# Optimization experiments

Hardware: AMD Instinct MI355X
Metric: run time of the kernel (lower is better)

Reference implementation:

```python
import jax, jax.numpy as jnp
import numpy as np

N_NODES = 50000
N_EDGES = 800000
D = 128


def _gcn_conv(x, edge_index, W, b):
    """PyG GCNConv: out = D^{-1/2} (A + I) D^{-1/2} (x W) + b.

    edge_index[0] = source nodes, edge_index[1] = target nodes.
    Self-loops handled analytically instead of materializing them.
    """
    n = x.shape[0]
    src, dst = edge_index[0], edge_index[1]
    h = x @ W  # [N, out]
    # degree with self-loop: in-degree of target + 1
    deg = jax.ops.segment_sum(jnp.ones_like(dst, dtype=h.dtype), dst, num_segments=n) + 1.0
    dinv = jax.lax.rsqrt(deg)  # deg >= 1, safe
    norm = dinv[src] * dinv[dst]  # [E]
    msgs = norm[:, None] * h[src]  # [E, out]  (the big irregular-gather intermediate)
    agg = jax.ops.segment_sum(msgs, dst, num_segments=n)
    # self-loop contribution: norm = dinv[i]*dinv[i] = 1/deg
    agg = agg + h * (1.0 / deg)[:, None]
    return agg + b


def setup_inputs() -> dict:
    key = jax.random.key(0)
    k1, k2, k3, k4 = jax.random.split(key, 4)
    x = jax.random.normal(k1, (N_NODES, D), dtype=jnp.float32)
    edge_index = jax.random.randint(k2, (2, N_EDGES), 0, N_NODES, dtype=jnp.int64)
    scale = 1.0 / np.sqrt(D)
    W1 = jax.random.normal(k3, (D, D), dtype=jnp.float32) * scale
    W2 = jax.random.normal(k4, (D, D), dtype=jnp.float32) * scale
    b1 = jnp.zeros((D,), dtype=jnp.float32)
    b2 = jnp.zeros((D,), dtype=jnp.float32)
    return {"x": x, "edge_index": edge_index, "W1": W1, "b1": b1, "W2": W2, "b2": b2}


def reference(x, edge_index, W1, b1, W2, b2):
    h = _gcn_conv(x, edge_index, W1, b1)
    h = jax.nn.relu(h)  # dropout p=0.0 -> identity
    out = _gcn_conv(h, edge_index, W2, b2)
    return out
```

## Files before the change

### kernel.cpp

```cpp
#include <hip/hip_runtime.h>

#define DF 128
#define NBKT_MAX 256
#define CAP 8192

typedef unsigned int uint;
typedef unsigned short ushort;
typedef __attribute__((ext_vector_type(8))) short short8;
typedef __attribute__((ext_vector_type(4))) float f32x4;

union frag_u { uint4 u4; short8 s8; };

__device__ __forceinline__ uint f2u(float f) { return __float_as_uint(f); }
__device__ __forceinline__ ushort rne_bf16(float v) {
    uint u = __float_as_uint(v);
    u = u + 0x7FFFu + ((u >> 16) & 1u);
    return (ushort)(u >> 16);
}
__device__ __forceinline__ float bflo(uint u) { return __uint_as_float(u << 16); }
__device__ __forceinline__ float bfhi(uint u) { return __uint_as_float(u & 0xFFFF0000u); }

__global__ __launch_bounds__(256) void scatter_wprep(const int* __restrict__ src,
                                                     const int* __restrict__ dst,
                                                     int* __restrict__ ccur,
                                                     uint* __restrict__ ebuf,
                                                     int E, int NB, int SB,
                                                     const float* __restrict__ W1,
                                                     const float* __restrict__ W2,
                                                     uint4* __restrict__ Whi,
                                                     uint4* __restrict__ Wlo) {
    __shared__ int cnt[NBKT_MAX];
    __shared__ int base[NBKT_MAX];
    int t = threadIdx.x;
    if ((int)blockIdx.x < SB) {
        int e0 = blockIdx.x * 8192, e1 = min(E, e0 + 8192);
        for (int i = t; i < NB; i += 256) cnt[i] = 0;
        __syncthreads();
        for (int e = e0 + t; e < e1; e += 256) atomicAdd(&cnt[dst[e] >> 8], 1);
        __syncthreads();
        for (int i = t; i < NB; i += 256) base[i] = cnt[i] ? atomicAdd(&ccur[i], cnt[i]) : 0;
        __syncthreads();
        for (int e = e0 + t; e < e1; e += 256) {
            int d = dst[e];
            int b = d >> 8;
            int pos = atomicAdd(&base[b], 1);
            if (pos < CAP) ebuf[(size_t)b * CAP + pos] = ((uint)(d & 255) << 24) | (uint)src[e];
        }
    } else {
        int tt4 = ((int)blockIdx.x - SB) * 256 + t;
        int wsel = tt4 >> 11;
        int tt = tt4 & 2047;
        const float* W = wsel ? W2 : W1;
        int lane = tt & 63;
        int n  = ((tt >> 6) & 7) * 16 + (lane & 15);
        int k0 = (tt >> 9) * 32 + (lane >> 4) * 8;
        uint hi[4], lo[4];
#pragma unroll
        for (int p = 0; p < 4; ++p) {
            float f0 = W[(size_t)(k0 + 2 * p) * DF + n];
            float f1 = W[(size_t)(k0 + 2 * p + 1) * DF + n];
            uint u0 = f2u(f0), u1 = f2u(f1);
            hi[p] = (u1 & 0xFFFF0000u) | (u0 >> 16);
            float l0 = f0 - __uint_as_float(u0 & 0xFFFF0000u);
            float l1 = f1 - __uint_as_float(u1 & 0xFFFF0000u);
            lo[p] = (f2u(l1) & 0xFFFF0000u) | (f2u(l0) >> 16);
        }
        Whi[wsel * 2048 + tt] = make_uint4(hi[0], hi[1], hi[2], hi[3]);
        Wlo[wsel * 2048 + tt] = make_uint4(lo[0], lo[1], lo[2], lo[3]);
    }
}

__global__ __launch_bounds__(256) void bucket_sort(const uint* __restrict__ ebuf,
                                                   const int* __restrict__ ccur,
                                                   int* __restrict__ rstart,
                                                   int* __restrict__ rend,
                                                   float* __restrict__ dinv,
                                                   ushort* __restrict__ srcs,
                                                   int N) {
    __shared__ int cnt[256];
    __shared__ int sp[256];
    int t = threadIdx.x, b = blockIdx.x;
    int count = min(ccur[b], CAP);
    const uint* eb = ebuf + (size_t)b * CAP;
    cnt[t] = 0;
    __syncthreads();
    for (int j = t; j < count; j += 256) atomicAdd(&cnt[eb[j] >> 24], 1);
    __syncthreads();
    int v = cnt[t];
    sp[t] = v;
    __syncthreads();
    for (int off = 1; off < 256; off <<= 1) {
        int x = (t >= off) ? sp[t - off] : 0;
        __syncthreads();
        sp[t] += x;
        __syncthreads();
    }
    int ex = sp[t] - v;
    int node = b * 256 + t;
    if (node < N) {
        rstart[node] = b * CAP + ex;
        rend[node]   = b * CAP + ex + v;
        dinv[node] = rsqrtf((float)v + 1.0f);
    }
    sp[t] = ex;
    __syncthreads();
    for (int j = t; j < count; j += 256) {
        uint e = eb[j];
        int pos = atomicAdd(&sp[e >> 24], 1);
        srcs[(size_t)b * CAP + pos] = (ushort)(e & 0xFFFFFFu);
    }
}

__global__ __launch_bounds__(256) void gemm_f32A(const float* __restrict__ A,
                                                 const uint4* __restrict__ Bhi,
                                                 const uint4* __restrict__ Blo,
                                                 const float* __restrict__ dinv,
                                                 ushort* __restrict__ Hq, int M) {
    const int lane = threadIdx.x & 63;
    const int w = threadIdx.x >> 6;
    const int l15 = lane & 15, quad = lane >> 4;
    const int rowbase = blockIdx.x * 128 + w * 32;

    f32x4 acc[2][8];
#pragma unroll
    for (int rt = 0; rt < 2; ++rt)
#pragma unroll
        for (int ct = 0; ct < 8; ++ct) acc[rt][ct] = (f32x4){0.f, 0.f, 0.f, 0.f};

    for (int q = 0; q < 4; ++q) {
        frag_u ah[2], al[2];
#pragma unroll
        for (int rt = 0; rt < 2; ++rt) {
            int m = rowbase + rt * 16 + l15;
            if (m >= M) m = M - 1;
            const float* ap = A + (size_t)m * DF + q * 32 + quad * 8;
            float4 v0 = *(const float4*)ap;
            float4 v1 = *(const float4*)(ap + 4);
            float f[8] = {v0.x, v0.y, v0.z, v0.w, v1.x, v1.y, v1.z, v1.w};
            uint hi[4], lo[4];
#pragma unroll
            for (int p = 0; p < 4; ++p) {
                uint u0 = f2u(f[2 * p]), u1 = f2u(f[2 * p + 1]);
                hi[p] = (u1 & 0xFFFF0000u) | (u0 >> 16);
                float l0 = f[2 * p]     - __uint_as_float(u0 & 0xFFFF0000u);
                float l1 = f[2 * p + 1] - __uint_as_float(u1 & 0xFFFF0000u);
                lo[p] = (f2u(l1) & 0xFFFF0000u) | (f2u(l0) >> 16);
            }
            ah[rt].u4 = make_uint4(hi[0], hi[1], hi[2], hi[3]);
            al[rt].u4 = make_uint4(lo[0], lo[1], lo[2], lo[3]);
        }
#pragma unroll
        for (int ct = 0; ct < 8; ++ct) {
            frag_u bh, bl;
            bh.u4 = Bhi[(q * 8 + ct) * 64 + lane];
            bl.u4 = Blo[(q * 8 + ct) * 64 + lane];
#pragma unroll
            for (int rt = 0; rt < 2; ++rt) {
                acc[rt][ct] = __builtin_amdgcn_mfma_f32_16x16x32_bf16(al[rt].s8, bh.s8, acc[rt][ct], 0, 0, 0);
                acc[rt][ct] = __builtin_amdgcn_mfma_f32_16x16x32_bf16(ah[rt].s8, bl.s8, acc[rt][ct], 0, 0, 0);
                acc[rt][ct] = __builtin_amdgcn_mfma_f32_16x16x32_bf16(ah[rt].s8, bh.s8, acc[rt][ct], 0, 0, 0);
            }
        }
    }
#pragma unroll
    for (int rt = 0; rt < 2; ++rt)
#pragma unroll
        for (int reg = 0; reg < 4; ++reg) {
            int row = rowbase + rt * 16 + quad * 4 + reg;
            if (row < M) {
                float di = dinv[row];
#pragma unroll
                for (int ct = 0; ct < 8; ++ct)
                    Hq[((size_t)(ct >> 1) * M + row) * 32 + (ct & 1) * 16 + l15] =
                        rne_bf16(acc[rt][ct][reg] * di);
            }
        }
}

__global__ __launch_bounds__(256) void gemm_bf16A(const ushort* __restrict__ A,
                                                  const uint4* __restrict__ Bhi,
                                                  const uint4* __restrict__ Blo,
                                                  const float* __restrict__ dinv,
                                                  ushort* __restrict__ Hq, int M) {
    const int lane = threadIdx.x & 63;
    const int w = threadIdx.x >> 6;
    const int l15 = lane & 15, quad = lane >> 4;
    const int rowbase = blockIdx.x * 128 + w * 32;

    f32x4 acc[2][8];
#pragma unroll
    for (int rt = 0; rt < 2; ++rt)
#pragma unroll
        for (int ct = 0; ct < 8; ++ct) acc[rt][ct] = (f32x4){0.f, 0.f, 0.f, 0.f};

    for (int q = 0; q < 4; ++q) {
        frag_u a[2];
#pragma unroll
        for (int rt = 0; rt < 2; ++rt) {
            int m = rowbase + rt * 16 + l15;
            if (m >= M) m = M - 1;
            const ushort* ap = A + ((size_t)q * M + m) * 32 + quad * 8;
            a[rt].u4 = *(const uint4*)ap;
        }
#pragma unroll
        for (int ct = 0; ct < 8; ++ct) {
            frag_u bh, bl;
            bh.u4 = Bhi[(q * 8 + ct) * 64 + lane];
            bl.u4 = Blo[(q * 8 + ct) * 64 + lane];
#pragma unroll
            for (int rt = 0; rt < 2; ++rt) {
                acc[rt][ct] = __builtin_amdgcn_mfma_f32_16x16x32_bf16(a[rt].s8, bl.s8, acc[rt][ct], 0, 0, 0);
                acc[rt][ct] = __builtin_amdgcn_mfma_f32_16x16x32_bf16(a[rt].s8, bh.s8, acc[rt][ct], 0, 0, 0);
            }
        }
    }
#pragma unroll
    for (int rt = 0; rt < 2; ++rt)
#pragma unroll
        for (int reg = 0; reg < 4; ++reg) {
            int row = rowbase + rt * 16 + quad * 4 + reg;
            if (row < M) {
                float di = dinv[row];
#pragma unroll
                for (int ct = 0; ct < 8; ++ct)
                    Hq[((size_t)(ct >> 1) * M + row) * 32 + (ct & 1) * 16 + l15] =
                        rne_bf16(acc[rt][ct][reg] * di);
            }
        }
}

template<bool L1>
__global__ __launch_bounds__(256) void quarter_gather(const uint4* __restrict__ H4,
                                                      const float* __restrict__ dinv,
                                                      const int* __restrict__ rstart,
                                                      const int* __restrict__ rend,
                                                      const ushort* __restrict__ srcs,
                                                      const float* __restrict__ bias,
                                                      void* __restrict__ outv, int N) {
    int t = threadIdx.x;
    int bid = blockIdx.x;
    int sub = bid & 7;
    int q = sub >> 1;
    int n = (bid >> 3) * 128 + (sub & 1) * 64 + (t >> 2);
    if (n >= N) return;
    int l = t & 3;
    const uint4* Hq4 = H4 + (size_t)q * N * 4;

    float4 bb0 = ((const float4*)bias)[q * 8 + l * 2];
    float4 bb1 = ((const float4*)bias)[q * 8 + l * 2 + 1];

    uint4 self = Hq4[(size_t)n * 4 + l];
    float a0 = bflo(self.x), a1 = bfhi(self.x), a2 = bflo(self.y), a3 = bfhi(self.y);
    float a4 = bflo(self.z), a5 = bfhi(self.z), a6 = bflo(self.w), a7 = bfhi(self.w);

    int j = rstart[n], end = rend[n];
    for (; j + 4 <= end; j += 4) {
        int s0 = srcs[j], s1 = srcs[j + 1], s2 = srcs[j + 2], s3 = srcs[j + 3];
        uint4 v0 = Hq4[(size_t)s0 * 4 + l];
        uint4 v1 = Hq4[(size_t)s1 * 4 + l];
        uint4 v2 = Hq4[(size_t)s2 * 4 + l];
        uint4 v3 = Hq4[(size_t)s3 * 4 + l];
        a0 += (bflo(v0.x) + bflo(v1.x)) + (bflo(v2.x) + bflo(v3.x));
        a1 += (bfhi(v0.x) + bfhi(v1.x)) + (bfhi(v2.x) + bfhi(v3.x));
        a2 += (bflo(v0.y) + bflo(v1.y)) + (bflo(v2.y) + bflo(v3.y));
        a3 += (bfhi(v0.y) + bfhi(v1.y)) + (bfhi(v2.y) + bfhi(v3.y));
        a4 += (bflo(v0.z) + bflo(v1.z)) + (bflo(v2.z) + bflo(v3.z));
        a5 += (bfhi(v0.z) + bfhi(v1.z)) + (bfhi(v2.z) + bfhi(v3.z));
        a6 += (bflo(v0.w) + bflo(v1.w)) + (bflo(v2.w) + bflo(v3.w));
        a7 += (bfhi(v0.w) + bfhi(v1.w)) + (bfhi(v2.w) + bfhi(v3.w));
    }
    for (; j < end; ++j) {
        uint4 v = Hq4[(size_t)srcs[j] * 4 + l];
        a0 += bflo(v.x); a1 += bfhi(v.x); a2 += bflo(v.y); a3 += bfhi(v.y);
        a4 += bflo(v.z); a5 += bfhi(v.z); a6 += bflo(v.w); a7 += bfhi(v.w);
    }
    float di = dinv[n];
    float o0 = fmaf(a0, di, bb0.x), o1 = fmaf(a1, di, bb0.y);
    float o2 = fmaf(a2, di, bb0.z), o3 = fmaf(a3, di, bb0.w);
    float o4 = fmaf(a4, di, bb1.x), o5 = fmaf(a5, di, bb1.y);
    float o6 = fmaf(a6, di, bb1.z), o7 = fmaf(a7, di, bb1.w);
    if (L1) {
        o0 = fmaxf(o0, 0.f); o1 = fmaxf(o1, 0.f); o2 = fmaxf(o2, 0.f); o3 = fmaxf(o3, 0.f);
        o4 = fmaxf(o4, 0.f); o5 = fmaxf(o5, 0.f); o6 = fmaxf(o6, 0.f); o7 = fmaxf(o7, 0.f);
        uint4 pk;
        pk.x = (uint)rne_bf16(o0) | ((uint)rne_bf16(o1) << 16);
        pk.y = (uint)rne_bf16(o2) | ((uint)rne_bf16(o3) << 16);
        pk.z = (uint)rne_bf16(o4) | ((uint)rne_bf16(o5) << 16);
        pk.w = (uint)rne_bf16(o6) | ((uint)rne_bf16(o7) << 16);
        ((uint4*)outv)[((size_t)q * N + n) * 4 + l] = pk;
    } else {
        float4* op = (float4*)((float*)outv + (size_t)n * DF + q * 32 + l * 8);
        op[0] = make_float4(o0, o1, o2, o3);
        op[1] = make_float4(o4, o5, o6, o7);
    }
}

extern "C" void kernel_launch(void* const* d_in, const int* in_sizes, int n_in,
                              void* d_out, int out_size, void* d_ws, size_t ws_size,
                              hipStream_t stream) {
    const float* x  = (const float*)d_in[0];
    const int*   ei = (const int*)d_in[1];
    const float* W1 = (const float*)d_in[2];
    const float* b1 = (const float*)d_in[3];
    const float* W2 = (const float*)d_in[4];
    const float* b2 = (const float*)d_in[5];

    const int N = in_sizes[0] / DF;
    const int E = in_sizes[1] / 2;
    const int* src = ei;
    const int* dstp = ei + E;
    const int NB = (N + 255) >> 8;
    const int SB = (E + 8191) / 8192;

    float* out = (float*)d_out;
    char* ws = (char*)d_ws;
    size_t off = 0;
    auto carve = [&](size_t bytes) { void* p = ws + off; off += (bytes + 255) & ~(size_t)255; return p; };
    ushort* Hq     = (ushort*)carve((size_t)N * DF * sizeof(ushort));
    ushort* Z1     = (ushort*)carve((size_t)N * DF * sizeof(ushort));
    float*  dinv   = (float*)carve((size_t)N * sizeof(float));
    int*    rstart = (int*)carve((size_t)N * sizeof(int));
    int*    rend   = (int*)carve((size_t)N * sizeof(int));
    uint*   ebuf   = (uint*)carve((size_t)NB * CAP * sizeof(uint));
    ushort* srcs   = (ushort*)carve((size_t)NB * CAP * sizeof(ushort));
    int*    ccur   = (int*)carve(NBKT_MAX * sizeof(int));
    uint4*  Whi    = (uint4*)carve(2 * 2048 * sizeof(uint4));
    uint4*  Wlo    = (uint4*)carve(2 * 2048 * sizeof(uint4));

    const int gemm_b = (N + 127) / 128;
    const int gath_b = ((N + 127) / 128) * 8;

    hipMemsetAsync(ccur, 0, NBKT_MAX * sizeof(int), stream);
    scatter_wprep<<<SB + 16, 256, 0, stream>>>(src, dstp, ccur, ebuf, E, NB, SB, W1, W2, Whi, Wlo);
    bucket_sort<<<NB, 256, 0, stream>>>(ebuf, ccur, rstart, rend, dinv, srcs, N);

    gemm_f32A<<<gemm_b, 256, 0, stream>>>(x, Whi, Wlo, dinv, Hq, N);
    quarter_gather<true><<<gath_b, 256, 0, stream>>>((const uint4*)Hq, dinv, rstart, rend, srcs, b1, Z1, N);

    gemm_bf16A<<<gemm_b, 256, 0, stream>>>(Z1, Whi + 2048, Wlo + 2048, dinv, Hq, N);
    quarter_gather<false><<<gath_b, 256, 0, stream>>>((const uint4*)Hq, dinv, rstart, rend, srcs, b2, out, N);
}
```

Baseline: 208.8 us.

## Fuse bucket sort with first GEMM and order gather nodes by degree

```diff
diff --git a/kernel.cpp b/kernel.cpp
--- a/kernel.cpp
+++ b/kernel.cpp
@@ -70,111 +70,122 @@
     }
 }
 
-__global__ __launch_bounds__(256) void bucket_sort(const uint* __restrict__ ebuf,
-                                                   const int* __restrict__ ccur,
-                                                   int* __restrict__ rstart,
-                                                   int* __restrict__ rend,
-                                                   float* __restrict__ dinv,
-                                                   ushort* __restrict__ srcs,
-                                                   int N) {
+__global__ __launch_bounds__(256) void sort_gemm1(const uint* __restrict__ ebuf,
+                                                  const int* __restrict__ ccur,
+                                                  int* __restrict__ rstart,
+                                                  int* __restrict__ rend,
+                                                  float* __restrict__ dinv,
+                                                  ushort* __restrict__ srcs,
+                                                  int* __restrict__ perm,
+                                                  const float* __restrict__ A,
+                                                  const uint4* __restrict__ Bhi,
+                                                  const uint4* __restrict__ Blo,
+                                                  ushort* __restrict__ Hq,
+                                                  int NB, int N) {
     __shared__ int cnt[256];
     __shared__ int sp[256];
-    int t = threadIdx.x, b = blockIdx.x;
-    int count = min(ccur[b], CAP);
-    const uint* eb = ebuf + (size_t)b * CAP;
-    cnt[t] = 0;
-    __syncthreads();
-    for (int j = t; j < count; j += 256) atomicAdd(&cnt[eb[j] >> 24], 1);
-    __syncthreads();
-    int v = cnt[t];
-    sp[t] = v;
-    __syncthreads();
-    for (int off = 1; off < 256; off <<= 1) {
-        int x = (t >= off) ? sp[t - off] : 0;
-        __syncthreads();
-        sp[t] += x;
-        __syncthreads();
-    }
-    int ex = sp[t] - v;
-    int node = b * 256 + t;
-    if (node < N) {
-        rstart[node] = b * CAP + ex;
-        rend[node]   = b * CAP + ex + v;
-        dinv[node] = rsqrtf((float)v + 1.0f);
-    }
-    sp[t] = ex;
-    __syncthreads();
-    for (int j = t; j < count; j += 256) {
-        uint e = eb[j];
-        int pos = atomicAdd(&sp[e >> 24], 1);
-        srcs[(size_t)b * CAP + pos] = (ushort)(e & 0xFFFFFFu);
-    }
-}
-
-__global__ __launch_bounds__(256) void gemm_f32A(const float* __restrict__ A,
-                                                 const uint4* __restrict__ Bhi,
-                                                 const uint4* __restrict__ Blo,
-                                                 const float* __restrict__ dinv,
-                                                 ushort* __restrict__ Hq, int M) {
-    const int lane = threadIdx.x & 63;
-    const int w = threadIdx.x >> 6;
-    const int l15 = lane & 15, quad = lane >> 4;
-    const int rowbase = blockIdx.x * 128 + w * 32;
-
-    f32x4 acc[2][8];
-#pragma unroll
-    for (int rt = 0; rt < 2; ++rt)
-#pragma unroll
-        for (int ct = 0; ct < 8; ++ct) acc[rt][ct] = (f32x4){0.f, 0.f, 0.f, 0.f};
-
-    for (int q = 0; q < 4; ++q) {
-        frag_u ah[2], al[2];
-#pragma unroll
-        for (int rt = 0; rt < 2; ++rt) {
-            int m = rowbase + rt * 16 + l15;
-            if (m >= M) m = M - 1;
-            const float* ap = A + (size_t)m * DF + q * 32 + quad * 8;
-            float4 v0 = *(const float4*)ap;
-            float4 v1 = *(const float4*)(ap + 4);
-            float f[8] = {v0.x, v0.y, v0.z, v0.w, v1.x, v1.y, v1.z, v1.w};
-            uint hi[4], lo[4];
-#pragma unroll
-            for (int p = 0; p < 4; ++p) {
-                uint u0 = f2u(f[2 * p]), u1 = f2u(f[2 * p + 1]);
-                hi[p] = (u1 & 0xFFFF0000u) | (u0 >> 16);
-                float l0 = f[2 * p]     - __uint_as_float(u0 & 0xFFFF0000u);
-                float l1 = f[2 * p + 1] - __uint_as_float(u1 & 0xFFFF0000u);
-                lo[p] = (f2u(l1) & 0xFFFF0000u) | (f2u(l0) >> 16);
-            }
-            ah[rt].u4 = make_uint4(hi[0], hi[1], hi[2], hi[3]);
-            al[rt].u4 = make_uint4(lo[0], lo[1], lo[2], lo[3]);
-        }
-#pragma unroll
-        for (int ct = 0; ct < 8; ++ct) {
-            frag_u bh, bl;
-            bh.u4 = Bhi[(q * 8 + ct) * 64 + lane];
-            bl.u4 = Blo[(q * 8 + ct) * 64 + lane];
+    __shared__ ushort prm[256];
+    int t = threadIdx.x;
+    if ((int)blockIdx.x < NB) {
+        int b = blockIdx.x;
+        int count = min(ccur[b], CAP);
+        const uint* eb = ebuf + (size_t)b * CAP;
+        cnt[t] = 0;
+        __syncthreads();
+        for (int j = t; j < count; j += 256) atomicAdd(&cnt[eb[j] >> 24], 1);
+        __syncthreads();
+        int v = cnt[t];
+        sp[t] = v;
+        __syncthreads();
+        for (int off = 1; off < 256; off <<= 1) {
+            int x = (t >= off) ? sp[t - off] : 0;
+            __syncthreads();
+            sp[t] += x;
+            __syncthreads();
+        }
+        int ex = sp[t] - v;
+        int node = b * 256 + t;
+        if (node < N) {
+            rstart[node] = b * CAP + ex;
+            rend[node]   = b * CAP + ex + v;
+            dinv[node] = rsqrtf((float)v + 1.0f);
+        }
+        int rank = 0;
+#pragma unroll 8
+        for (int u = 0; u < 256; ++u) {
+            int du = cnt[u];
+            rank += (du > v) || (du == v && u < t);
+        }
+        prm[rank] = (ushort)t;
+        sp[t] = ex;
+        __syncthreads();
+        perm[b * 256 + t] = b * 256 + (int)prm[t];
+        for (int j = t; j < count; j += 256) {
+            uint e = eb[j];
+            int pos = atomicAdd(&sp[e >> 24], 1);
+            srcs[(size_t)b * CAP + pos] = (ushort)(e & 0xFFFFFFu);
+        }
+    } else {
+        const int lane = t & 63;
+        const int w = t >> 6;
+        const int l15 = lane & 15, quad = lane >> 4;
+        const int rowbase = ((int)blockIdx.x - NB) * 128 + w * 32;
+        const int M = N;
+
+        f32x4 acc[2][8];
+#pragma unroll
+        for (int rt = 0; rt < 2; ++rt)
+#pragma unroll
+            for (int ct = 0; ct < 8; ++ct) acc[rt][ct] = (f32x4){0.f, 0.f, 0.f, 0.f};
+
+        for (int q = 0; q < 4; ++q) {
+            frag_u ah[2], al[2];
 #pragma unroll
             for (int rt = 0; rt < 2; ++rt) {
-                acc[rt][ct] = __builtin_amdgcn_mfma_f32_16x16x32_bf16(al[rt].s8, bh.s8, acc[rt][ct], 0, 0, 0);
-                acc[rt][ct] = __builtin_amdgcn_mfma_f32_16x16x32_bf16(ah[rt].s8, bl.s8, acc[rt][ct], 0, 0, 0);
-                acc[rt][ct] = __builtin_amdgcn_mfma_f32_16x16x32_bf16(ah[rt].s8, bh.s8, acc[rt][ct], 0, 0, 0);
-            }
-        }
-    }
-#pragma unroll
-    for (int rt = 0; rt < 2; ++rt)
-#pragma unroll
-        for (int reg = 0; reg < 4; ++reg) {
-            int row = rowbase + rt * 16 + quad * 4 + reg;
-            if (row < M) {
-                float di = dinv[row];
-#pragma unroll
-                for (int ct = 0; ct < 8; ++ct)
-                    Hq[((size_t)(ct >> 1) * M + row) * 32 + (ct & 1) * 16 + l15] =
-                        rne_bf16(acc[rt][ct][reg] * di);
-            }
-        }
+                int m = rowbase + rt * 16 + l15;
+                if (m >= M) m = M - 1;
+                const float* ap = A + (size_t)m * DF + q * 32 + quad * 8;
+                float4 v0 = *(const float4*)ap;
+                float4 v1 = *(const float4*)(ap + 4);
+                float f[8] = {v0.x, v0.y, v0.z, v0.w, v1.x, v1.y, v1.z, v1.w};
+                uint hi[4], lo[4];
+#pragma unroll
+                for (int p = 0; p < 4; ++p) {
+                    uint u0 = f2u(f[2 * p]), u1 = f2u(f[2 * p + 1]);
+                    hi[p] = (u1 & 0xFFFF0000u) | (u0 >> 16);
+                    float l0 = f[2 * p]     - __uint_as_float(u0 & 0xFFFF0000u);
+                    float l1 = f[2 * p + 1] - __uint_as_float(u1 & 0xFFFF0000u);
+                    lo[p] = (f2u(l1) & 0xFFFF0000u) | (f2u(l0) >> 16);
+                }
+                ah[rt].u4 = make_uint4(hi[0], hi[1], hi[2], hi[3]);
+                al[rt].u4 = make_uint4(lo[0], lo[1], lo[2], lo[3]);
+            }
+#pragma unroll
+            for (int ct = 0; ct < 8; ++ct) {
+                frag_u bh, bl;
+                bh.u4 = Bhi[(q * 8 + ct) * 64 + lane];
+                bl.u4 = Blo[(q * 8 + ct) * 64 + lane];
+#pragma unroll
+                for (int rt = 0; rt < 2; ++rt) {
+                    acc[rt][ct] = __builtin_amdgcn_mfma_f32_16x16x32_bf16(al[rt].s8, bh.s8, acc[rt][ct], 0, 0, 0);
+                    acc[rt][ct] = __builtin_amdgcn_mfma_f32_16x16x32_bf16(ah[rt].s8, bl.s8, acc[rt][ct], 0, 0, 0);
+                    acc[rt][ct] = __builtin_amdgcn_mfma_f32_16x16x32_bf16(ah[rt].s8, bh.s8, acc[rt][ct], 0, 0, 0);
+                }
+            }
+        }
+#pragma unroll
+        for (int rt = 0; rt < 2; ++rt)
+#pragma unroll
+            for (int reg = 0; reg < 4; ++reg) {
+                int row = rowbase + rt * 16 + quad * 4 + reg;
+                if (row < M) {
+#pragma unroll
+                    for (int ct = 0; ct < 8; ++ct)
+                        Hq[((size_t)(ct >> 1) * M + row) * 32 + (ct & 1) * 16 + l15] =
+                            rne_bf16(acc[rt][ct][reg]);
+                }
+            }
+    }
 }
 
 __global__ __launch_bounds__(256) void gemm_bf16A(const ushort* __restrict__ A,
@@ -235,13 +246,15 @@
                                                       const int* __restrict__ rstart,
                                                       const int* __restrict__ rend,
                                                       const ushort* __restrict__ srcs,
+                                                      const int* __restrict__ perm,
                                                       const float* __restrict__ bias,
                                                       void* __restrict__ outv, int N) {
     int t = threadIdx.x;
     int bid = blockIdx.x;
     int sub = bid & 7;
     int q = sub >> 1;
-    int n = (bid >> 3) * 128 + (sub & 1) * 64 + (t >> 2);
+    int slot = (bid >> 3) * 128 + (sub & 1) * 64 + (t >> 2);
+    int n = perm[slot];
     if (n >= N) return;
     int l = t & 3;
     const uint4* Hq4 = H4 + (size_t)q * N * 4;
@@ -249,9 +262,11 @@
     float4 bb0 = ((const float4*)bias)[q * 8 + l * 2];
     float4 bb1 = ((const float4*)bias)[q * 8 + l * 2 + 1];
 
+    float di = dinv[n];
     uint4 self = Hq4[(size_t)n * 4 + l];
-    float a0 = bflo(self.x), a1 = bfhi(self.x), a2 = bflo(self.y), a3 = bfhi(self.y);
-    float a4 = bflo(self.z), a5 = bfhi(self.z), a6 = bflo(self.w), a7 = bfhi(self.w);
+    float sc = L1 ? di : 1.0f;
+    float a0 = bflo(self.x) * sc, a1 = bfhi(self.x) * sc, a2 = bflo(self.y) * sc, a3 = bfhi(self.y) * sc;
+    float a4 = bflo(self.z) * sc, a5 = bfhi(self.z) * sc, a6 = bflo(self.w) * sc, a7 = bfhi(self.w) * sc;
 
     int j = rstart[n], end = rend[n];
     for (; j + 4 <= end; j += 4) {
@@ -260,21 +275,49 @@
         uint4 v1 = Hq4[(size_t)s1 * 4 + l];
         uint4 v2 = Hq4[(size_t)s2 * 4 + l];
         uint4 v3 = Hq4[(size_t)s3 * 4 + l];
-        a0 += (bflo(v0.x) + bflo(v1.x)) + (bflo(v2.x) + bflo(v3.x));
-        a1 += (bfhi(v0.x) + bfhi(v1.x)) + (bfhi(v2.x) + bfhi(v3.x));
-        a2 += (bflo(v0.y) + bflo(v1.y)) + (bflo(v2.y) + bflo(v3.y));
-        a3 += (bfhi(v0.y) + bfhi(v1.y)) + (bfhi(v2.y) + bfhi(v3.y));
-        a4 += (bflo(v0.z) + bflo(v1.z)) + (bflo(v2.z) + bflo(v3.z));
-        a5 += (bfhi(v0.z) + bfhi(v1.z)) + (bfhi(v2.z) + bfhi(v3.z));
-        a6 += (bflo(v0.w) + bflo(v1.w)) + (bflo(v2.w) + bflo(v3.w));
-        a7 += (bfhi(v0.w) + bfhi(v1.w)) + (bfhi(v2.w) + bfhi(v3.w));
+        if constexpr (L1) {
+            float d0 = dinv[s0], d1 = dinv[s1], d2 = dinv[s2], d3 = dinv[s3];
+            a0 = fmaf(bflo(v0.x), d0, a0); a0 = fmaf(bflo(v1.x), d1, a0);
+            a0 = fmaf(bflo(v2.x), d2, a0); a0 = fmaf(bflo(v3.x), d3, a0);
+            a1 = fmaf(bfhi(v0.x), d0, a1); a1 = fmaf(bfhi(v1.x), d1, a1);
+            a1 = fmaf(bfhi(v2.x), d2, a1); a1 = fmaf(bfhi(v3.x), d3, a1);
+            a2 = fmaf(bflo(v0.y), d0, a2); a2 = fmaf(bflo(v1.y), d1, a2);
+            a2 = fmaf(bflo(v2.y), d2, a2); a2 = fmaf(bflo(v3.y), d3, a2);
+            a3 = fmaf(bfhi(v0.y), d0, a3); a3 = fmaf(bfhi(v1.y), d1, a3);
+            a3 = fmaf(bfhi(v2.y), d2, a3); a3 = fmaf(bfhi(v3.y), d3, a3);
+            a4 = fmaf(bflo(v0.z), d0, a4); a4 = fmaf(bflo(v1.z), d1, a4);
+            a4 = fmaf(bflo(v2.z), d2, a4); a4 = fmaf(bflo(v3.z), d3, a4);
+            a5 = fmaf(bfhi(v0.z), d0, a5); a5 = fmaf(bfhi(v1.z), d1, a5);
+            a5 = fmaf(bfhi(v2.z), d2, a5); a5 = fmaf(bfhi(v3.z), d3, a5);
+            a6 = fmaf(bflo(v0.w), d0, a6); a6 = fmaf(bflo(v1.w), d1, a6);
+            a6 = fmaf(bflo(v2.w), d2, a6); a6 = fmaf(bflo(v3.w), d3, a6);
+            a7 = fmaf(bfhi(v0.w), d0, a7); a7 = fmaf(bfhi(v1.w), d1, a7);
+            a7 = fmaf(bfhi(v2.w), d2, a7); a7 = fmaf(bfhi(v3.w), d3, a7);
+        } else {
+            a0 += (bflo(v0.x) + bflo(v1.x)) + (bflo(v2.x) + bflo(v3.x));
+            a1 += (bfhi(v0.x) + bfhi(v1.x)) + (bfhi(v2.x) + bfhi(v3.x));
+            a2 += (bflo(v0.y) + bflo(v1.y)) + (bflo(v2.y) + bflo(v3.y));
+            a3 += (bfhi(v0.y) + bfhi(v1.y)) + (bfhi(v2.y) + bfhi(v3.y));
+            a4 += (bflo(v0.z) + bflo(v1.z)) + (bflo(v2.z) + bflo(v3.z));
+            a5 += (bfhi(v0.z) + bfhi(v1.z)) + (bfhi(v2.z) + bfhi(v3.z));
+            a6 += (bflo(v0.w) + bflo(v1.w)) + (bflo(v2.w) + bflo(v3.w));
+            a7 += (bfhi(v0.w) + bfhi(v1.w)) + (bfhi(v2.w) + bfhi(v3.w));
+        }
     }
     for (; j < end; ++j) {
-        uint4 v = Hq4[(size_t)srcs[j] * 4 + l];
-        a0 += bflo(v.x); a1 += bfhi(v.x); a2 += bflo(v.y); a3 += bfhi(v.y);
-        a4 += bflo(v.z); a5 += bfhi(v.z); a6 += bflo(v.w); a7 += bfhi(v.w);
-    }
-    float di = dinv[n];
+        int s = srcs[j];
+        uint4 v = Hq4[(size_t)s * 4 + l];
+        if constexpr (L1) {
+            float d = dinv[s];
+            a0 = fmaf(bflo(v.x), d, a0); a1 = fmaf(bfhi(v.x), d, a1);
+            a2 = fmaf(bflo(v.y), d, a2); a3 = fmaf(bfhi(v.y), d, a3);
+            a4 = fmaf(bflo(v.z), d, a4); a5 = fmaf(bfhi(v.z), d, a5);
+            a6 = fmaf(bflo(v.w), d, a6); a7 = fmaf(bfhi(v.w), d, a7);
+        } else {
+            a0 += bflo(v.x); a1 += bfhi(v.x); a2 += bflo(v.y); a3 += bfhi(v.y);
+            a4 += bflo(v.z); a5 += bfhi(v.z); a6 += bflo(v.w); a7 += bfhi(v.w);
+        }
+    }
     float o0 = fmaf(a0, di, bb0.x), o1 = fmaf(a1, di, bb0.y);
     float o2 = fmaf(a2, di, bb0.z), o3 = fmaf(a3, di, bb0.w);
     float o4 = fmaf(a4, di, bb1.x), o5 = fmaf(a5, di, bb1.y);
@@ -321,6 +364,7 @@
     float*  dinv   = (float*)carve((size_t)N * sizeof(float));
     int*    rstart = (int*)carve((size_t)N * sizeof(int));
     int*    rend   = (int*)carve((size_t)N * sizeof(int));
+    int*    perm   = (int*)carve((size_t)NB * 256 * sizeof(int));
     uint*   ebuf   = (uint*)carve((size_t)NB * CAP * sizeof(uint));
     ushort* srcs   = (ushort*)carve((size_t)NB * CAP * sizeof(ushort));
     int*    ccur   = (int*)carve(NBKT_MAX * sizeof(int));
@@ -332,11 +376,14 @@
 
     hipMemsetAsync(ccur, 0, NBKT_MAX * sizeof(int), stream);
     scatter_wprep<<<SB + 16, 256, 0, stream>>>(src, dstp, ccur, ebuf, E, NB, SB, W1, W2, Whi, Wlo);
-    bucket_sort<<<NB, 256, 0, stream>>>(ebuf, ccur, rstart, rend, dinv, srcs, N);
-
-    gemm_f32A<<<gemm_b, 256, 0, stream>>>(x, Whi, Wlo, dinv, Hq, N);
-    quarter_gather<true><<<gath_b, 256, 0, stream>>>((const uint4*)Hq, dinv, rstart, rend, srcs, b1, Z1, N);
+
+    sort_gemm1<<<NB + gemm_b, 256, 0, stream>>>(ebuf, ccur, rstart, rend, dinv, srcs, perm,
+                                                x, Whi, Wlo, Hq, NB, N);
+
+    quarter_gather<true><<<gath_b, 256, 0, stream>>>((const uint4*)Hq, dinv, rstart, rend,
+                                                     srcs, perm, b1, Z1, N);
 
     gemm_bf16A<<<gemm_b, 256, 0, stream>>>(Z1, Whi + 2048, Wlo + 2048, dinv, Hq, N);
-    quarter_gather<false><<<gath_b, 256, 0, stream>>>((const uint4*)Hq, dinv, rstart, rend, srcs, b2, out, N);
-}
+    quarter_gather<false><<<gath_b, 256, 0, stream>>>((const uint4*)Hq, dinv, rstart, rend,
+                                                      srcs, perm, b2, out, N);
+}
```

Result: slower. 234.9 us (+12.5%).

## Fuse bucket sort with first GEMM and vectorize gather index loads

Applied to the files above, without the earlier changes.

```diff
diff --git a/kernel.cpp b/kernel.cpp
--- a/kernel.cpp
+++ b/kernel.cpp
@@ -23,6 +23,7 @@
 __global__ __launch_bounds__(256) void scatter_wprep(const int* __restrict__ src,
                                                      const int* __restrict__ dst,
                                                      int* __restrict__ ccur,
+                                                     int* __restrict__ deg,
                                                      uint* __restrict__ ebuf,
                                                      int E, int NB, int SB,
                                                      const float* __restrict__ W1,
@@ -36,7 +37,11 @@
         int e0 = blockIdx.x * 8192, e1 = min(E, e0 + 8192);
         for (int i = t; i < NB; i += 256) cnt[i] = 0;
         __syncthreads();
-        for (int e = e0 + t; e < e1; e += 256) atomicAdd(&cnt[dst[e] >> 8], 1);
+        for (int e = e0 + t; e < e1; e += 256) {
+            int d = dst[e];
+            atomicAdd(&deg[d], 1);
+            atomicAdd(&cnt[d >> 8], 1);
+        }
         __syncthreads();
         for (int i = t; i < NB; i += 256) base[i] = cnt[i] ? atomicAdd(&ccur[i], cnt[i]) : 0;
         __syncthreads();
@@ -70,111 +75,115 @@
     }
 }
 
-__global__ __launch_bounds__(256) void bucket_sort(const uint* __restrict__ ebuf,
-                                                   const int* __restrict__ ccur,
-                                                   int* __restrict__ rstart,
-                                                   int* __restrict__ rend,
-                                                   float* __restrict__ dinv,
-                                                   ushort* __restrict__ srcs,
-                                                   int N) {
+__global__ __launch_bounds__(256) void sort_gemm1(const uint* __restrict__ ebuf,
+                                                  const int* __restrict__ ccur,
+                                                  int* __restrict__ rstart,
+                                                  int* __restrict__ rend,
+                                                  float* __restrict__ dinv,
+                                                  ushort* __restrict__ srcs,
+                                                  const int* __restrict__ deg,
+                                                  const float* __restrict__ A,
+                                                  const uint4* __restrict__ Bhi,
+                                                  const uint4* __restrict__ Blo,
+                                                  ushort* __restrict__ Hq,
+                                                  int NB, int N) {
     __shared__ int cnt[256];
     __shared__ int sp[256];
-    int t = threadIdx.x, b = blockIdx.x;
-    int count = min(ccur[b], CAP);
-    const uint* eb = ebuf + (size_t)b * CAP;
-    cnt[t] = 0;
-    __syncthreads();
-    for (int j = t; j < count; j += 256) atomicAdd(&cnt[eb[j] >> 24], 1);
-    __syncthreads();
-    int v = cnt[t];
-    sp[t] = v;
-    __syncthreads();
-    for (int off = 1; off < 256; off <<= 1) {
-        int x = (t >= off) ? sp[t - off] : 0;
-        __syncthreads();
-        sp[t] += x;
-        __syncthreads();
-    }
-    int ex = sp[t] - v;
-    int node = b * 256 + t;
-    if (node < N) {
-        rstart[node] = b * CAP + ex;
-        rend[node]   = b * CAP + ex + v;
-        dinv[node] = rsqrtf((float)v + 1.0f);
-    }
-    sp[t] = ex;
-    __syncthreads();
-    for (int j = t; j < count; j += 256) {
-        uint e = eb[j];
-        int pos = atomicAdd(&sp[e >> 24], 1);
-        srcs[(size_t)b * CAP + pos] = (ushort)(e & 0xFFFFFFu);
-    }
-}
-
-__global__ __launch_bounds__(256) void gemm_f32A(const float* __restrict__ A,
-                                                 const uint4* __restrict__ Bhi,
-                                                 const uint4* __restrict__ Blo,
-                                                 const float* __restrict__ dinv,
-                                                 ushort* __restrict__ Hq, int M) {
-    const int lane = threadIdx.x & 63;
-    const int w = threadIdx.x >> 6;
-    const int l15 = lane & 15, quad = lane >> 4;
-    const int rowbase = blockIdx.x * 128 + w * 32;
-
-    f32x4 acc[2][8];
-#pragma unroll
-    for (int rt = 0; rt < 2; ++rt)
-#pragma unroll
-        for (int ct = 0; ct < 8; ++ct) acc[rt][ct] = (f32x4){0.f, 0.f, 0.f, 0.f};
-
-    for (int q = 0; q < 4; ++q) {
-        frag_u ah[2], al[2];
-#pragma unroll
-        for (int rt = 0; rt < 2; ++rt) {
-            int m = rowbase + rt * 16 + l15;
-            if (m >= M) m = M - 1;
-            const float* ap = A + (size_t)m * DF + q * 32 + quad * 8;
-            float4 v0 = *(const float4*)ap;
-            float4 v1 = *(const float4*)(ap + 4);
-            float f[8] = {v0.x, v0.y, v0.z, v0.w, v1.x, v1.y, v1.z, v1.w};
-            uint hi[4], lo[4];
-#pragma unroll
-            for (int p = 0; p < 4; ++p) {
-                uint u0 = f2u(f[2 * p]), u1 = f2u(f[2 * p + 1]);
-                hi[p] = (u1 & 0xFFFF0000u) | (u0 >> 16);
-                float l0 = f[2 * p]     - __uint_as_float(u0 & 0xFFFF0000u);
-                float l1 = f[2 * p + 1] - __uint_as_float(u1 & 0xFFFF0000u);
-                lo[p] = (f2u(l1) & 0xFFFF0000u) | (f2u(l0) >> 16);
-            }
-            ah[rt].u4 = make_uint4(hi[0], hi[1], hi[2], hi[3]);
-            al[rt].u4 = make_uint4(lo[0], lo[1], lo[2], lo[3]);
-        }
-#pragma unroll
-        for (int ct = 0; ct < 8; ++ct) {
-            frag_u bh, bl;
-            bh.u4 = Bhi[(q * 8 + ct) * 64 + lane];
-            bl.u4 = Blo[(q * 8 + ct) * 64 + lane];
+    int t = threadIdx.x;
+    if ((int)blockIdx.x < NB) {
+        int b = blockIdx.x;
+        int count = min(ccur[b], CAP);
+        const uint* eb = ebuf + (size_t)b * CAP;
+        cnt[t] = 0;
+        __syncthreads();
+        for (int j = t; j < count; j += 256) atomicAdd(&cnt[eb[j] >> 24], 1);
+        __syncthreads();
+        int v = cnt[t];
+        int pv = (v + 7) & ~7;
+        sp[t] = pv;
+        __syncthreads();
+        for (int off = 1; off < 256; off <<= 1) {
+            int x = (t >= off) ? sp[t - off] : 0;
+            __syncthreads();
+            sp[t] += x;
+            __syncthreads();
+        }
+        int ex = sp[t] - pv;
+        int node = b * 256 + t;
+        if (node < N) {
+            rstart[node] = b * CAP + ex;
+            rend[node]   = b * CAP + ex + v;
+            dinv[node] = rsqrtf((float)v + 1.0f);
+        }
+        sp[t] = ex;
+        __syncthreads();
+        for (int j = t; j < count; j += 256) {
+            uint e = eb[j];
+            int pos = atomicAdd(&sp[e >> 24], 1);
+            if (pos < CAP) srcs[(size_t)b * CAP + pos] = (ushort)(e & 0xFFFFFFu);
+        }
+    } else {
+        const int lane = t & 63;
+        const int w = t >> 6;
+        const int l15 = lane & 15, quad = lane >> 4;
+        const int rowbase = ((int)blockIdx.x - NB) * 128 + w * 32;
+        const int M = N;
+
+        f32x4 acc[2][8];
+#pragma unroll
+        for (int rt = 0; rt < 2; ++rt)
+#pragma unroll
+            for (int ct = 0; ct < 8; ++ct) acc[rt][ct] = (f32x4){0.f, 0.f, 0.f, 0.f};
+
+        for (int q = 0; q < 4; ++q) {
+            frag_u ah[2], al[2];
 #pragma unroll
             for (int rt = 0; rt < 2; ++rt) {
-                acc[rt][ct] = __builtin_amdgcn_mfma_f32_16x16x32_bf16(al[rt].s8, bh.s8, acc[rt][ct], 0, 0, 0);
-                acc[rt][ct] = __builtin_amdgcn_mfma_f32_16x16x32_bf16(ah[rt].s8, bl.s8, acc[rt][ct], 0, 0, 0);
-                acc[rt][ct] = __builtin_amdgcn_mfma_f32_16x16x32_bf16(ah[rt].s8, bh.s8, acc[rt][ct], 0, 0, 0);
-            }
-        }
-    }
-#pragma unroll
-    for (int rt = 0; rt < 2; ++rt)
-#pragma unroll
-        for (int reg = 0; reg < 4; ++reg) {
-            int row = rowbase + rt * 16 + quad * 4 + reg;
-            if (row < M) {
-                float di = dinv[row];
-#pragma unroll
-                for (int ct = 0; ct < 8; ++ct)
-                    Hq[((size_t)(ct >> 1) * M + row) * 32 + (ct & 1) * 16 + l15] =
-                        rne_bf16(acc[rt][ct][reg] * di);
-            }
-        }
+                int m = rowbase + rt * 16 + l15;
+                if (m >= M) m = M - 1;
+                const float* ap = A + (size_t)m * DF + q * 32 + quad * 8;
+                float4 v0 = *(const float4*)ap;
+                float4 v1 = *(const float4*)(ap + 4);
+                float f[8] = {v0.x, v0.y, v0.z, v0.w, v1.x, v1.y, v1.z, v1.w};
+                uint hi[4], lo[4];
+#pragma unroll
+                for (int p = 0; p < 4; ++p) {
+                    uint u0 = f2u(f[2 * p]), u1 = f2u(f[2 * p + 1]);
+                    hi[p] = (u1 & 0xFFFF0000u) | (u0 >> 16);
+                    float l0 = f[2 * p]     - __uint_as_float(u0 & 0xFFFF0000u);
+                    float l1 = f[2 * p + 1] - __uint_as_float(u1 & 0xFFFF0000u);
+                    lo[p] = (f2u(l1) & 0xFFFF0000u) | (f2u(l0) >> 16);
+                }
+                ah[rt].u4 = make_uint4(hi[0], hi[1], hi[2], hi[3]);
+                al[rt].u4 = make_uint4(lo[0], lo[1], lo[2], lo[3]);
+            }
+#pragma unroll
+            for (int ct = 0; ct < 8; ++ct) {
+                frag_u bh, bl;
+                bh.u4 = Bhi[(q * 8 + ct) * 64 + lane];
+                bl.u4 = Blo[(q * 8 + ct) * 64 + lane];
+#pragma unroll
+                for (int rt = 0; rt < 2; ++rt) {
+                    acc[rt][ct] = __builtin_amdgcn_mfma_f32_16x16x32_bf16(al[rt].s8, bh.s8, acc[rt][ct], 0, 0, 0);
+                    acc[rt][ct] = __builtin_amdgcn_mfma_f32_16x16x32_bf16(ah[rt].s8, bl.s8, acc[rt][ct], 0, 0, 0);
+                    acc[rt][ct] = __builtin_amdgcn_mfma_f32_16x16x32_bf16(ah[rt].s8, bh.s8, acc[rt][ct], 0, 0, 0);
+                }
+            }
+        }
+#pragma unroll
+        for (int rt = 0; rt < 2; ++rt)
+#pragma unroll
+            for (int reg = 0; reg < 4; ++reg) {
+                int row = rowbase + rt * 16 + quad * 4 + reg;
+                if (row < M) {
+                    float di = rsqrtf((float)deg[row] + 1.0f);
+#pragma unroll
+                    for (int ct = 0; ct < 8; ++ct)
+                        Hq[((size_t)(ct >> 1) * M + row) * 32 + (ct & 1) * 16 + l15] =
+                            rne_bf16(acc[rt][ct][reg] * di);
+                }
+            }
+    }
 }
 
 __global__ __launch_bounds__(256) void gemm_bf16A(const ushort* __restrict__ A,
@@ -254,20 +263,36 @@
     float a4 = bflo(self.z), a5 = bfhi(self.z), a6 = bflo(self.w), a7 = bfhi(self.w);
 
     int j = rstart[n], end = rend[n];
-    for (; j + 4 <= end; j += 4) {
-        int s0 = srcs[j], s1 = srcs[j + 1], s2 = srcs[j + 2], s3 = srcs[j + 3];
+    for (; j + 8 <= end; j += 8) {
+        uint4 sv = *(const uint4*)(srcs + j);
+        int s0 = sv.x & 0xFFFF, s1 = sv.x >> 16;
+        int s2 = sv.y & 0xFFFF, s3 = sv.y >> 16;
+        int s4 = sv.z & 0xFFFF, s5 = sv.z >> 16;
+        int s6 = sv.w & 0xFFFF, s7 = sv.w >> 16;
         uint4 v0 = Hq4[(size_t)s0 * 4 + l];
         uint4 v1 = Hq4[(size_t)s1 * 4 + l];
         uint4 v2 = Hq4[(size_t)s2 * 4 + l];
         uint4 v3 = Hq4[(size_t)s3 * 4 + l];
-        a0 += (bflo(v0.x) + bflo(v1.x)) + (bflo(v2.x) + bflo(v3.x));
-        a1 += (bfhi(v0.x) + bfhi(v1.x)) + (bfhi(v2.x) + bfhi(v3.x));
-        a2 += (bflo(v0.y) + bflo(v1.y)) + (bflo(v2.y) + bflo(v3.y));
-        a3 += (bfhi(v0.y) + bfhi(v1.y)) + (bfhi(v2.y) + bfhi(v3.y));
-        a4 += (bflo(v0.z) + bflo(v1.z)) + (bflo(v2.z) + bflo(v3.z));
-        a5 += (bfhi(v0.z) + bfhi(v1.z)) + (bfhi(v2.z) + bfhi(v3.z));
-        a6 += (bflo(v0.w) + bflo(v1.w)) + (bflo(v2.w) + bflo(v3.w));
-        a7 += (bfhi(v0.w) + bfhi(v1.w)) + (bfhi(v2.w) + bfhi(v3.w));
+        uint4 v4 = Hq4[(size_t)s4 * 4 + l];
+        uint4 v5 = Hq4[(size_t)s5 * 4 + l];
+        uint4 v6 = Hq4[(size_t)s6 * 4 + l];
+        uint4 v7 = Hq4[(size_t)s7 * 4 + l];
+        a0 += ((bflo(v0.x) + bflo(v1.x)) + (bflo(v2.x) + bflo(v3.x)))
+            + ((bflo(v4.x) + bflo(v5.x)) + (bflo(v6.x) + bflo(v7.x)));
+        a1 += ((bfhi(v0.x) + bfhi(v1.x)) + (bfhi(v2.x) + bfhi(v3.x)))
+            + ((bfhi(v4.x) + bfhi(v5.x)) + (bfhi(v6.x) + bfhi(v7.x)));
+        a2 += ((bflo(v0.y) + bflo(v1.y)) + (bflo(v2.y) + bflo(v3.y)))
+            + ((bflo(v4.y) + bflo(v5.y)) + (bflo(v6.y) + bflo(v7.y)));
+        a3 += ((bfhi(v0.y) + bfhi(v1.y)) + (bfhi(v2.y) + bfhi(v3.y)))
+            + ((bfhi(v4.y) + bfhi(v5.y)) + (bfhi(v6.y) + bfhi(v7.y)));
+        a4 += ((bflo(v0.z) + bflo(v1.z)) + (bflo(v2.z) + bflo(v3.z)))
+            + ((bflo(v4.z) + bflo(v5.z)) + (bflo(v6.z) + bflo(v7.z)));
+        a5 += ((bfhi(v0.z) + bfhi(v1.z)) + (bfhi(v2.z) + bfhi(v3.z)))
+            + ((bfhi(v4.z) + bfhi(v5.z)) + (bfhi(v6.z) + bfhi(v7.z)));
+        a6 += ((bflo(v0.w) + bflo(v1.w)) + (bflo(v2.w) + bflo(v3.w)))
+            + ((bflo(v4.w) + bflo(v5.w)) + (bflo(v6.w) + bflo(v7.w)));
+        a7 += ((bfhi(v0.w) + bfhi(v1.w)) + (bfhi(v2.w) + bfhi(v3.w)))
+            + ((bfhi(v4.w) + bfhi(v5.w)) + (bfhi(v6.w) + bfhi(v7.w)));
     }
     for (; j < end; ++j) {
         uint4 v = Hq4[(size_t)srcs[j] * 4 + l];
@@ -324,19 +349,23 @@
     uint*   ebuf   = (uint*)carve((size_t)NB * CAP * sizeof(uint));
     ushort* srcs   = (ushort*)carve((size_t)NB * CAP * sizeof(ushort));
     int*    ccur   = (int*)carve(NBKT_MAX * sizeof(int));
+    int*    deg    = (int*)carve((size_t)N * sizeof(int));
     uint4*  Whi    = (uint4*)carve(2 * 2048 * sizeof(uint4));
     uint4*  Wlo    = (uint4*)carve(2 * 2048 * sizeof(uint4));
 
     const int gemm_b = (N + 127) / 128;
     const int gath_b = ((N + 127) / 128) * 8;
 
-    hipMemsetAsync(ccur, 0, NBKT_MAX * sizeof(int), stream);
-    scatter_wprep<<<SB + 16, 256, 0, stream>>>(src, dstp, ccur, ebuf, E, NB, SB, W1, W2, Whi, Wlo);
-    bucket_sort<<<NB, 256, 0, stream>>>(ebuf, ccur, rstart, rend, dinv, srcs, N);
-
-    gemm_f32A<<<gemm_b, 256, 0, stream>>>(x, Whi, Wlo, dinv, Hq, N);
-    quarter_gather<true><<<gath_b, 256, 0, stream>>>((const uint4*)Hq, dinv, rstart, rend, srcs, b1, Z1, N);
+    hipMemsetAsync(ccur, 0, NBKT_MAX * sizeof(int) + (size_t)N * sizeof(int), stream);
+    scatter_wprep<<<SB + 16, 256, 0, stream>>>(src, dstp, ccur, deg, ebuf, E, NB, SB, W1, W2, Whi, Wlo);
+
+    sort_gemm1<<<NB + gemm_b, 256, 0, stream>>>(ebuf, ccur, rstart, rend, dinv, srcs, deg,
+                                                x, Whi, Wlo, Hq, NB, N);
+
+    quarter_gather<true><<<gath_b, 256, 0, stream>>>((const uint4*)Hq, dinv, rstart, rend,
+                                                     srcs, b1, Z1, N);
 
     gemm_bf16A<<<gemm_b, 256, 0, stream>>>(Z1, Whi + 2048, Wlo + 2048, dinv, Hq, N);
-    quarter_gather<false><<<gath_b, 256, 0, stream>>>((const uint4*)Hq, dinv, rstart, rend, srcs, b2, out, N);
-}
+    quarter_gather<false><<<gath_b, 256, 0, stream>>>((const uint4*)Hq, dinv, rstart, rend,
+                                                      srcs, b2, out, N);
+}
```

New measurement: 235.7 us. +12.9%, slower.
